# Kernel tuning notes

Hardware: AMD Instinct MI355X
Metric: run time of the kernel (lower is better)

The kernel has to match this reference:

```python
import jax, jax.numpy as jnp
import numpy as np

C = 512; H = 64; W = 64; STRIDE = 16; NA = 9; IMG = 1024
PRE_NMS = 6000; POST_NMS = 300; NMS_T = 0.7; MIN_SIZE = 16.0
BBOX_CLIP = float(np.log(1000.0 / 16.0))  # standard dw/dh clamp for exp() safety


def _make_anchors():
    # 3 scales x 3 aspect ratios on a stride-16 grid -> (H*W*9, 4) xyxy anchors
    scales = np.array([128.0, 256.0, 512.0])
    ratios = np.array([0.5, 1.0, 2.0])
    hs = (scales[:, None] * np.sqrt(ratios)[None, :]).ravel()
    ws = (scales[:, None] / np.sqrt(ratios)[None, :]).ravel()
    yy, xx = np.meshgrid((np.arange(H) + 0.5) * STRIDE, (np.arange(W) + 0.5) * STRIDE, indexing='ij')
    ctr = np.stack([xx.ravel(), yy.ravel()], -1)            # (HW, 2) centers
    wh = np.stack([ws, hs], -1)                              # (9, 2)
    anc = np.concatenate([ctr[:, None, :] - 0.5 * wh[None], ctr[:, None, :] + 0.5 * wh[None]], -1)
    return anc.reshape(-1, 4).astype(np.float32)             # (HW*9, 4)


def setup_inputs() -> dict:
    key = jax.random.key(0)
    k = jax.random.split(key, 4)
    return {
        'feature_map': jax.random.normal(k[0], (1, C, H, W), jnp.float32),
        'anchors': jnp.asarray(_make_anchors()),
        'image_shape': jnp.array([IMG, IMG], jnp.int32),
        'conv1_w': 0.01 * jax.random.normal(k[1], (C, C, 3, 3), jnp.float32),
        'conv1_b': jnp.zeros((C,), jnp.float32),
        'cls_w': 0.01 * jax.random.normal(k[2], (NA, C, 1, 1), jnp.float32),
        'cls_b': jnp.zeros((NA,), jnp.float32),
        'box_w': 0.01 * jax.random.normal(k[3], (NA * 4, C, 1, 1), jnp.float32),
        'box_b': jnp.zeros((NA * 4,), jnp.float32),
    }


def _conv(x, w, b):
    dn = ('NCHW', 'OIHW', 'NCHW')
    return jax.lax.conv_general_dilated(x, w, (1, 1), 'SAME', dimension_numbers=dn) + b[None, :, None, None]


def _decode_boxes(deltas, anchors):
    aw = anchors[:, 2] - anchors[:, 0]
    ah = anchors[:, 3] - anchors[:, 1]
    ax = anchors[:, 0] + 0.5 * aw
    ay = anchors[:, 1] + 0.5 * ah
    dx, dy, dw, dh = deltas[:, 0], deltas[:, 1], deltas[:, 2], deltas[:, 3]
    dw = jnp.minimum(dw, BBOX_CLIP)
    dh = jnp.minimum(dh, BBOX_CLIP)
    px = dx * aw + ax
    py = dy * ah + ay
    pw = jnp.exp(dw) * aw
    ph = jnp.exp(dh) * ah
    return jnp.stack([px - 0.5 * pw, py - 0.5 * ph, px + 0.5 * pw, py + 0.5 * ph], -1)


def _pairwise_iou(a, b):
    area_a = (a[:, 2] - a[:, 0]) * (a[:, 3] - a[:, 1])
    area_b = (b[:, 2] - b[:, 0]) * (b[:, 3] - b[:, 1])
    lt = jnp.maximum(a[:, None, :2], b[None, :, :2])
    rb = jnp.minimum(a[:, None, 2:], b[None, :, 2:])
    wh = jnp.clip(rb - lt, 0.0)
    inter = wh[..., 0] * wh[..., 1]
    union = area_a[:, None] + area_b[None, :] - inter
    return jnp.where(union > 0, inter / union, 0.0)


def reference(feature_map, anchors, image_shape, conv1_w, conv1_b, cls_w, cls_b, box_w, box_b):
    # conv head
    y = jax.nn.relu(_conv(feature_map, conv1_w, conv1_b))
    scores = _conv(y, cls_w, cls_b).reshape(-1)            # (H*W*9,)  torch .view(-1) order
    deltas = _conv(y, box_w, box_b).reshape(-1, 4)         # (H*W*9, 4) torch .reshape(-1,4) order
    preds = _decode_boxes(deltas, anchors)

    # filter_proposals: sigmoid -> topk 6000 -> clamp -> min-size -> NMS(0.7) -> top 300
    s = jax.nn.sigmoid(scores)
    topv, topi = jax.lax.top_k(s, PRE_NMS)                  # sorted descending
    b = preds[topi]
    h_img = image_shape[0].astype(jnp.float32)
    w_img = image_shape[1].astype(jnp.float32)
    b = jnp.stack([jnp.clip(b[:, 0], 0.0, w_img), jnp.clip(b[:, 1], 0.0, h_img),
                   jnp.clip(b[:, 2], 0.0, w_img), jnp.clip(b[:, 3], 0.0, h_img)], -1)
    valid = ((b[:, 2] - b[:, 0]) >= MIN_SIZE) & ((b[:, 3] - b[:, 1]) >= MIN_SIZE)

    iou = _pairwise_iou(b, b)                               # (6000, 6000)
    idx = jnp.arange(PRE_NMS)

    def body(i, keep):  # greedy NMS in score order (boxes already sorted desc)
        sup = (iou[i] > NMS_T) & keep[i] & (idx > i)
        return keep & (~sup)

    keep = jax.lax.fori_loop(0, PRE_NMS, body, valid)
    fs = jnp.where(keep, topv, -1.0)                        # suppressed/invalid -> sentinel
    sc, i2 = jax.lax.top_k(fs, POST_NMS)
    return b[i2], sc
```

## Files before the change

### kernel.cpp

```cpp
#include <hip/hip_runtime.h>
#include <hip/hip_bf16.h>

typedef unsigned int u32;
typedef unsigned long long u64;

#define OFF_Y      0ull
#define OFF_WT     8388608ull
#define OFF_ZPART  8388608ull
#define OFF_SCORES 11337728ull
#define OFF_DRAW   11485184ull
#define OFF_HIST   12075008ull
#define MEMSET_LEN 524288ull
#define OFF_TOPV   12665344ull
#define OFF_BOXES  12714496ull
#define OFF_VW     12812800ull
#define OFF_MASK   12813824ull

#define NS     36864
#define PRE    6000
#define POST   300
#define SORTN  8192
#define MROW   96

__global__ __launch_bounds__(256) void k_wtrans(const float* __restrict__ gw,
                                                float* __restrict__ wT) {
    int o = blockIdx.x * 256 + threadIdx.x;
    if (o >= 512 * 512 * 9) return;
    int ci = o / 4608;
    int r = o - ci * 4608;
    int co = r / 9;
    int k = r - co * 9;
    wT[o] = gw[(co * 512 + ci) * 9 + k];
}

#define CI 16
#define NROW 4
#define XROW 66
#define CHUNK_ELEMS (CI * NROW * XROW)
#define STAGE_IT 17
__global__ __launch_bounds__(256) void k_conv1(const float* __restrict__ x,
                                               const float* __restrict__ wT,
                                               const float* __restrict__ gb,
                                               float* __restrict__ y) {
    __shared__ float xs[CHUNK_ELEMS];
    const int t = threadIdx.x;
    const int tx = t & 63;
    const int wv = __builtin_amdgcn_readfirstlane(t >> 6);
    const int cob = (blockIdx.x & 15) << 5;
    const int h0 = (blockIdx.x >> 4) << 1;
    const int co_base = cob + (wv << 3);

    int offs[STAGE_IT];
    u32 vmask = 0;
#pragma unroll
    for (int u = 0; u < STAGE_IT; ++u) {
        int idx = t + u * 256;
        offs[u] = 0;
        if (idx < CHUNK_ELEMS) {
            int ci = idx / (NROW * XROW);
            int rem = idx - ci * (NROW * XROW);
            int row = rem / XROW;
            int col = rem - row * XROW;
            int gr = h0 + row - 1, gc = col - 1;
            if ((unsigned)gr < 64u && (unsigned)gc < 64u) {
                offs[u] = ci * 4096 + (gr << 6) + gc;
                vmask |= 1u << u;
            }
        }
    }

    float acc[8][2];
#pragma unroll
    for (int c = 0; c < 8; ++c) { acc[c][0] = 0.f; acc[c][1] = 0.f; }

    float st[STAGE_IT];
#pragma unroll
    for (int u = 0; u < STAGE_IT; ++u)
        st[u] = (vmask >> u & 1) ? x[offs[u]] : 0.f;

#pragma unroll 1
    for (int cc = 0; cc < 32; ++cc) {
        if (cc) __syncthreads();
#pragma unroll
        for (int u = 0; u < STAGE_IT; ++u) {
            int idx = t + u * 256;
            if (idx < CHUNK_ELEMS) xs[idx] = st[u];
        }
        __syncthreads();
        if (cc + 1 < 32) {
            const float* xsrc = x + (cc + 1) * CI * 4096;
#pragma unroll
            for (int u = 0; u < STAGE_IT; ++u)
                st[u] = (vmask >> u & 1) ? xsrc[offs[u]] : 0.f;
        }

        const int cig0 = cc * CI;
#pragma unroll 1
        for (int ci = 0; ci < CI; ++ci) {
            float xr[12];
            {
                const float* xp = xs + ci * (NROW * XROW) + tx;
#pragma unroll
                for (int r = 0; r < NROW; ++r) {
                    xr[r * 3 + 0] = xp[r * XROW + 0];
                    xr[r * 3 + 1] = xp[r * XROW + 1];
                    xr[r * 3 + 2] = xp[r * XROW + 2];
                }
            }
            const float* wbase = wT + ((size_t)(cig0 + ci) * 512 + co_base) * 9;
            {
                float4 wq[9];
                const float4* wp = (const float4*)wbase;
#pragma unroll
                for (int i = 0; i < 9; ++i) wq[i] = wp[i];
                const float* w = (const float*)wq;
#pragma unroll
                for (int co = 0; co < 4; ++co)
#pragma unroll
                    for (int k = 0; k < 9; ++k) {
                        const int kh = k / 3, kw = k - kh * 3;
                        float wv_ = w[co * 9 + k];
                        acc[co][0] += wv_ * xr[(0 + kh) * 3 + kw];
                        acc[co][1] += wv_ * xr[(1 + kh) * 3 + kw];
                    }
            }
            {
                float4 wq[9];
                const float4* wp = (const float4*)(wbase + 36);
#pragma unroll
                for (int i = 0; i < 9; ++i) wq[i] = wp[i];
                const float* w = (const float*)wq;
#pragma unroll
                for (int co = 0; co < 4; ++co)
#pragma unroll
                    for (int k = 0; k < 9; ++k) {
                        const int kh = k / 3, kw = k - kh * 3;
                        float wv_ = w[co * 9 + k];
                        acc[co + 4][0] += wv_ * xr[(0 + kh) * 3 + kw];
                        acc[co + 4][1] += wv_ * xr[(1 + kh) * 3 + kw];
                    }
            }
        }
    }

#pragma unroll
    for (int co = 0; co < 8; ++co) {
        float bias = gb[co_base + co];
#pragma unroll
        for (int r = 0; r < 2; ++r) {
            float v = acc[co][r] + bias;
            v = v > 0.f ? v : 0.f;
            y[(co_base + co) * 4096 + ((h0 + r) << 6) + tx] = v;
        }
    }
}

__global__ __launch_bounds__(256) void k_heads_part(const float* __restrict__ y,
                                                    const float* __restrict__ cw,
                                                    const float* __restrict__ bw,
                                                    float* __restrict__ zpart) {
    __shared__ __align__(16) float ys[64][132];
    const int t = threadIdx.x;
    const int px = t & 63;
    const int gu = __builtin_amdgcn_readfirstlane(t >> 6);
    const int px0 = (blockIdx.x & 63) << 6;
    const int q = blockIdx.x >> 6;
    const int cib = q << 7;
    const int nch = (gu == 0) ? 12 : 11;

    const float* wrow[12];
#pragma unroll
    for (int j = 0; j < 12; ++j) {
        int ch = gu + 4 * j;
        if (ch < 9) wrow[j] = cw + ch * 512;
        else if (ch < 45) wrow[j] = bw + (ch - 9) * 512;
        else wrow[j] = cw;
    }
    float acc[12];
#pragma unroll
    for (int j = 0; j < 12; ++j) acc[j] = 0.f;

    for (int idx = t; idx < 128 * 64; idx += 256) {
        int ci = idx >> 6;
        int pp = idx & 63;
        ys[pp][ci] = y[(cib + ci) * 4096 + px0 + pp];
    }
    __syncthreads();

#pragma unroll 1
    for (int cq = 0; cq < 32; ++cq) {
        float4 yv = *(const float4*)&ys[px][cq << 2];
        float4 wv[12];
#pragma unroll
        for (int j = 0; j < 12; ++j)
            if (j < nch) wv[j] = *(const float4*)(wrow[j] + cib + (cq << 2));
#pragma unroll
        for (int j = 0; j < 12; ++j)
            if (j < nch)
                acc[j] += wv[j].x * yv.x + wv[j].y * yv.y + wv[j].z * yv.z + wv[j].w * yv.w;
    }
    for (int j = 0; j < nch; ++j) {
        int ch = gu + 4 * j;
        zpart[((q * 45 + ch) << 12) + px0 + px] = acc[j];
    }
}

__global__ __launch_bounds__(256) void k_hreduce(const float* __restrict__ zpart,
                                                 const float* __restrict__ cb,
                                                 const float* __restrict__ bb,
                                                 float* __restrict__ scores,
                                                 float* __restrict__ draw,
                                                 u32* __restrict__ hist) {
    int i = blockIdx.x * 256 + threadIdx.x;
    if (i >= 45 * 4096) return;
    int ch = i >> 12;
    int sp = i & 4095;
    float z = zpart[((0 * 45 + ch) << 12) + sp] + zpart[((1 * 45 + ch) << 12) + sp] +
              zpart[((2 * 45 + ch) << 12) + sp] + zpart[((3 * 45 + ch) << 12) + sp];
    if (ch < 9) {
        z += cb[ch];
        float s = 1.f / (1.f + expf(-z));
        scores[(ch << 12) + sp] = s;
        u32 sb = __float_as_uint(s);
        atomicAdd(&hist[sb >> 13], 1u);
    } else {
        z += bb[ch - 9];
        draw[((ch - 9) << 12) + sp] = z;
    }
}

__global__ __launch_bounds__(1024) void k_select(const u32* __restrict__ hist,
                                                 const float* __restrict__ scores,
                                                 const float* __restrict__ draw,
                                                 const float* __restrict__ anchors,
                                                 const int* __restrict__ ishape,
                                                 float* __restrict__ boxes,
                                                 float* __restrict__ topv,
                                                 u64* __restrict__ vw) {
    __shared__ u32 csum[1024];
    __shared__ u32 suf[1024];
    __shared__ u64 sk[SORTN];
    __shared__ int sel_s, cnt_s;
    const int t = threadIdx.x;

    u32 s = 0;
    const u32* hp = hist + t * 128;
    for (int i = 0; i < 128; ++i) s += hp[i];
    csum[t] = s;
    suf[t] = s;
    if (t == 0) cnt_s = 0;
    __syncthreads();
    for (int off = 1; off < 1024; off <<= 1) {
        u32 v = suf[t] + ((t + off < 1024) ? suf[t + off] : 0u);
        __syncthreads();
        suf[t] = v;
        __syncthreads();
    }
    u32 above = suf[t] - csum[t];
    if (above < (u32)PRE && suf[t] >= (u32)PRE) {
        u32 run = above;
        int bstar = t * 128;
        u32 found = 0;
        for (int b2 = 127; b2 >= 0; --b2) {
            u32 c = hp[b2];
            if (!found && run + c >= (u32)PRE) { bstar = t * 128 + b2; found = 1; }
            if (!found) run += c;
        }
        sel_s = bstar;
    }
    for (int i = t; i < SORTN; i += 1024) sk[i] = 0;
    __syncthreads();

    const int sel = sel_s;
    for (int i = t; i < NS; i += 1024) {
        u32 sb = __float_as_uint(scores[i]);
        if ((int)(sb >> 13) >= sel) {
            int p = atomicAdd(&cnt_s, 1);
            if (p < SORTN) sk[p] = ((u64)sb << 32) | (u32)(~i);
        }
    }
    __syncthreads();

    const int base = t << 3;
    u64 a[8];
    {
#pragma unroll
        for (int u = 0; u < 8; ++u) a[u] = sk[base + u];
#pragma unroll
        for (int k = 2; k <= 8; k <<= 1) {
#pragma unroll
            for (int j = k >> 1; j > 0; j >>= 1) {
#pragma unroll
                for (int u = 0; u < 8; ++u) {
                    if ((u & j) == 0) {
                        int l = u | j;
                        bool up = (((base + u) & k) == 0);
                        u64 x0 = a[u], x1 = a[l];
                        if (up ? (x0 < x1) : (x0 > x1)) { a[u] = x1; a[l] = x0; }
                    }
                }
            }
        }
#pragma unroll
        for (int u = 0; u < 8; ++u) sk[base + u] = a[u];
        __syncthreads();
    }
    for (int k = 16; k <= SORTN; k <<= 1) {
        for (int j = k >> 1; j >= 8; j >>= 1) {
#pragma unroll
            for (int s2 = 0; s2 < 4; ++s2) {
                int pidx = t + (s2 << 10);
                int i = ((pidx & ~(j - 1)) << 1) | (pidx & (j - 1));
                int l = i | j;
                u64 x0 = sk[i], x1 = sk[l];
                bool up = ((i & k) == 0);
                if (up ? (x0 < x1) : (x0 > x1)) { sk[i] = x1; sk[l] = x0; }
            }
            __syncthreads();
        }
#pragma unroll
        for (int u = 0; u < 8; ++u) a[u] = sk[base + u];
        {
            bool up = ((base & k) == 0);
#pragma unroll
            for (int j = 4; j > 0; j >>= 1) {
#pragma unroll
                for (int u = 0; u < 8; ++u) {
                    if ((u & j) == 0) {
                        int l = u | j;
                        u64 x0 = a[u], x1 = a[l];
                        if (up ? (x0 < x1) : (x0 > x1)) { a[u] = x1; a[l] = x0; }
                    }
                }
            }
        }
#pragma unroll
        for (int u = 0; u < 8; ++u) sk[base + u] = a[u];
        __syncthreads();
    }

    const float wimg = (float)ishape[1], himg = (float)ishape[0];
#pragma unroll 1
    for (int s2 = 0; s2 < 6; ++s2) {
        int r = (s2 << 10) + t;
        bool valid = false;
        if (r < PRE) {
            u64 key = sk[r];
            u32 sb = (u32)(key >> 32);
            int i = (int)(~(u32)key);
            topv[r] = __uint_as_float(sb);
            int c = i >> 10;
            int t4 = i & 1023;
            float4 d4 = *(const float4*)(draw + c * 4096 + (t4 << 2));
            float4 a4 = *(const float4*)(anchors + i * 4);
            float aw = a4.z - a4.x, ah = a4.w - a4.y;
            float ax = a4.x + 0.5f * aw, ay = a4.y + 0.5f * ah;
            const float CLIPV = (float)4.135166556742356;
            float dw = fminf(d4.z, CLIPV);
            float dh = fminf(d4.w, CLIPV);
            float px = d4.x * aw + ax, py = d4.y * ah + ay;
            float pw = expf(dw) * aw, ph = expf(dh) * ah;
            float x1 = fminf(fmaxf(px - 0.5f * pw, 0.f), wimg);
            float y1 = fminf(fmaxf(py - 0.5f * ph, 0.f), himg);
            float x2 = fminf(fmaxf(px + 0.5f * pw, 0.f), wimg);
            float y2 = fminf(fmaxf(py + 0.5f * ph, 0.f), himg);
            valid = (x2 - x1 >= 16.f) && (y2 - y1 >= 16.f);
            *(float4*)(boxes + r * 4) = make_float4(x1, y1, x2, y2);
        }
        u64 bm = __ballot(valid);
        if ((t & 63) == 0) vw[(s2 << 4) + (t >> 6)] = bm;
    }
}

__global__ __launch_bounds__(256) void k_mask(const float* __restrict__ boxes,
                                              u64* __restrict__ mask) {
    __shared__ float4 cbx[16 * 65];
    const int t = threadIdx.x;
    const int r0 = blockIdx.x << 4;
    const int row = r0 + (t >> 4);
    const int wloc = t & 15;
    float4 rb = *(const float4*)(boxes + row * 4);
    float area_a = (rb.z - rb.x) * (rb.w - rb.y);
    for (int chunk = 0; chunk < 6; ++chunk) {
        int j0c = chunk << 10;
        for (int idx = t; idx < 1024; idx += 256) {
            int j = j0c + idx;
            float4 v = make_float4(0.f, 0.f, 0.f, 0.f);
            if (j < PRE) v = *(const float4*)(boxes + j * 4);
            cbx[(idx >> 6) * 65 + (idx & 63)] = v;
        }
        __syncthreads();
        u64 bits = 0;
        const float4* cbr = cbx + wloc * 65;
        for (int b = 0; b < 64; ++b) {
            int j = j0c + (wloc << 6) + b;
            float4 ob = cbr[b];
            float area_b = (ob.z - ob.x) * (ob.w - ob.y);
            float ltx = fmaxf(rb.x, ob.x), lty = fmaxf(rb.y, ob.y);
            float rbx = fminf(rb.z, ob.z), rby = fminf(rb.w, ob.w);
            float wx = fmaxf(rbx - ltx, 0.f), wy = fmaxf(rby - lty, 0.f);
            float inter = wx * wy;
            float uni = area_a + area_b - inter;
            float iou = (uni > 0.f) ? (inter / uni) : 0.f;
            if (iou > 0.7f && j > row && j < PRE) bits |= (1ull << b);
        }
        mask[(size_t)row * MROW + (chunk << 4) + wloc] = bits;
        __syncthreads();
    }
}

__global__ __launch_bounds__(320) void k_nms_out(const u64* __restrict__ mask,
                                                 const u64* __restrict__ vw,
                                                 const float* __restrict__ boxes,
                                                 const float* __restrict__ topv,
                                                 float* __restrict__ out) {
    __shared__ u64 rem[MROW];
    __shared__ u64 rows16[16][MROW];
    __shared__ u64 kws[MROW];
    __shared__ int keepl[POST];
    const int tid = threadIdx.x;
    for (int i = tid; i < MROW; i += 320) { rem[i] = 0ull; kws[i] = 0ull; }
    __syncthreads();
    int kc = 0;
    bool done = false;
    for (int w = 0; w < 94 && !done; ++w) {
        u64 aw = vw[w] & ~rem[w];
        u64 kwbits = 0;
        while (aw != 0ull && !done) {
            int bq[16];
            u64 tmp = aw;
#pragma unroll
            for (int q2 = 0; q2 < 16; ++q2) {
                bq[q2] = tmp ? __builtin_ctzll(tmp) : 64;
                tmp &= tmp - 1;
            }
#pragma unroll
            for (int u = 0; u < 5; ++u) {
                int i = tid + u * 320;
                if (i < 16 * MROW) {
                    int q2 = i / MROW;
                    int ww = i - q2 * MROW;
                    if (bq[q2] < 64)
                        rows16[q2][ww] = mask[(size_t)((w << 6) + bq[q2]) * MROW + ww];
                }
            }
            __syncthreads();
            for (int q2 = 0; q2 < 16; ++q2) {
                int b = bq[q2];
                if (b >= 64) break;
                if (!((aw >> b) & 1ull)) continue;
                if (tid == 0) keepl[kc] = (w << 6) + b;
                kc++;
                kwbits |= (1ull << b);
                if (kc >= POST) { done = true; break; }
                if (tid < MROW) rem[tid] |= rows16[q2][tid];
                aw &= ~rows16[q2][w];
                aw &= ~(1ull << b);
            }
            __syncthreads();
        }
        if (tid == 0) kws[w] = kwbits;
        __syncthreads();
    }
    __syncthreads();

    int j = tid;
    if (j >= POST) return;
    int r;
    float sc;
    if (j < kc) {
        r = keepl[j];
        sc = topv[r];
    } else {
        int target = j - kc;
        r = PRE - 1;
        int cum = 0;
        for (int w = 0; w < 94; ++w) {
            u64 kb = kws[w];
            int nvalid = (w < 93) ? 64 : 48;
            u64 vmask2 = (nvalid == 64) ? ~0ull : ((1ull << nvalid) - 1ull);
            u64 nk = (~kb) & vmask2;
            int c = __popcll(nk);
            if (cum + c > target) {
                int need = target - cum;
                u64 m = nk;
                for (int q = 0; q < need; ++q) m &= (m - 1);
                r = (w << 6) + __builtin_ctzll(m);
                break;
            }
            cum += c;
        }
        sc = -1.0f;
    }
    out[j * 4 + 0] = boxes[r * 4 + 0];
    out[j * 4 + 1] = boxes[r * 4 + 1];
    out[j * 4 + 2] = boxes[r * 4 + 2];
    out[j * 4 + 3] = boxes[r * 4 + 3];
    out[1200 + j] = sc;
}

extern "C" void kernel_launch(void* const* d_in, const int* in_sizes, int n_in,
                              void* d_out, int out_size, void* d_ws, size_t ws_size,
                              hipStream_t stream) {
    const float* x = (const float*)d_in[0];
    const float* anchors = (const float*)d_in[1];
    const int* ishape = (const int*)d_in[2];
    const float* c1w = (const float*)d_in[3];
    const float* c1b = (const float*)d_in[4];
    const float* clw = (const float*)d_in[5];
    const float* clb = (const float*)d_in[6];
    const float* bxw = (const float*)d_in[7];
    const float* bxb = (const float*)d_in[8];

    char* ws = (char*)d_ws;
    float* y      = (float*)(ws + OFF_Y);
    float* wT     = (float*)(ws + OFF_WT);
    float* zpart  = (float*)(ws + OFF_ZPART);
    float* scores = (float*)(ws + OFF_SCORES);
    float* draw   = (float*)(ws + OFF_DRAW);
    u32*   hist   = (u32*)(ws + OFF_HIST);
    float* topv   = (float*)(ws + OFF_TOPV);
    float* boxes  = (float*)(ws + OFF_BOXES);
    u64*   vw     = (u64*)(ws + OFF_VW);
    u64*   mask   = (u64*)(ws + OFF_MASK);

    k_wtrans<<<(512 * 512 * 9 + 255) / 256, 256, 0, stream>>>(c1w, wT);
    k_conv1<<<512, 256, 0, stream>>>(x, wT, c1b, y);
    hipMemsetAsync(ws + OFF_HIST, 0, MEMSET_LEN, stream);
    k_heads_part<<<256, 256, 0, stream>>>(y, clw, bxw, zpart);
    k_hreduce<<<(45 * 4096 + 255) / 256, 256, 0, stream>>>(zpart, clb, bxb, scores, draw, hist);
    k_select<<<1, 1024, 0, stream>>>(hist, scores, draw, anchors, ishape, boxes, topv, vw);
    k_mask<<<PRE / 16, 256, 0, stream>>>(boxes, mask);
    k_nms_out<<<1, 320, 0, stream>>>(mask, vw, boxes, topv, (float*)d_out);
}
```

Baseline: 773.7 us.

## Restructure conv1 to one output row per block with packed FMA weights

The 3x3 conv is reworked so each block handles a single output row instead of two. The grid doubles to 1024 blocks and shared staging shrinks to 3 input rows. The weight transpose now puts the kernel tap outermost, so each thread loads 8 consecutive output-channel weights per tap as float4 pairs and accumulates with 2-wide vector FMAs, aiming at packed FP32 math and fewer loads; launch bounds also request higher occupancy. The histogram memset is folded into k_heads_part to drop a separate memset call. The trade-off is that input rows are now reused across only one output row, so more staged input is loaded per output.

```diff
diff --git a/kernel.cpp b/kernel.cpp
--- a/kernel.cpp
+++ b/kernel.cpp
@@ -3,6 +3,8 @@
 
 typedef unsigned int u32;
 typedef unsigned long long u64;
+typedef float v2f __attribute__((ext_vector_type(2)));
+typedef float v4f __attribute__((ext_vector_type(4)));
 
 #define OFF_Y      0ull
 #define OFF_WT     8388608ull
@@ -10,7 +12,6 @@
 #define OFF_SCORES 11337728ull
 #define OFF_DRAW   11485184ull
 #define OFF_HIST   12075008ull
-#define MEMSET_LEN 524288ull
 #define OFF_TOPV   12665344ull
 #define OFF_BOXES  12714496ull
 #define OFF_VW     12812800ull
@@ -28,26 +29,25 @@
     if (o >= 512 * 512 * 9) return;
     int ci = o / 4608;
     int r = o - ci * 4608;
-    int co = r / 9;
-    int k = r - co * 9;
-    wT[o] = gw[(co * 512 + ci) * 9 + k];
+    int k = r >> 9;
+    int co = r & 511;
+    wT[o] = gw[co * 4608 + ci * 9 + k];
 }
 
 #define CI 16
-#define NROW 4
 #define XROW 66
-#define CHUNK_ELEMS (CI * NROW * XROW)
-#define STAGE_IT 17
-__global__ __launch_bounds__(256) void k_conv1(const float* __restrict__ x,
-                                               const float* __restrict__ wT,
-                                               const float* __restrict__ gb,
-                                               float* __restrict__ y) {
+#define CHUNK_ELEMS (CI * 3 * XROW)
+#define STAGE_IT 13
+__global__ __launch_bounds__(256, 4) void k_conv1(const float* __restrict__ x,
+                                                  const float* __restrict__ wT,
+                                                  const float* __restrict__ gb,
+                                                  float* __restrict__ y) {
     __shared__ float xs[CHUNK_ELEMS];
     const int t = threadIdx.x;
     const int tx = t & 63;
     const int wv = __builtin_amdgcn_readfirstlane(t >> 6);
     const int cob = (blockIdx.x & 15) << 5;
-    const int h0 = (blockIdx.x >> 4) << 1;
+    const int h0 = blockIdx.x >> 4;
     const int co_base = cob + (wv << 3);
 
     int offs[STAGE_IT];
@@ -57,8 +57,8 @@
         int idx = t + u * 256;
         offs[u] = 0;
         if (idx < CHUNK_ELEMS) {
-            int ci = idx / (NROW * XROW);
-            int rem = idx - ci * (NROW * XROW);
+            int ci = idx / (3 * XROW);
+            int rem = idx - ci * (3 * XROW);
             int row = rem / XROW;
             int col = rem - row * XROW;
             int gr = h0 + row - 1, gc = col - 1;
@@ -69,9 +69,9 @@
         }
     }
 
-    float acc[8][2];
-#pragma unroll
-    for (int c = 0; c < 8; ++c) { acc[c][0] = 0.f; acc[c][1] = 0.f; }
+    v2f acc2[4];
+#pragma unroll
+    for (int j = 0; j < 4; ++j) acc2[j] = (v2f){0.f, 0.f};
 
     float st[STAGE_IT];
 #pragma unroll
@@ -95,72 +95,57 @@
         }
 
         const int cig0 = cc * CI;
-#pragma unroll 1
+#pragma unroll 2
         for (int ci = 0; ci < CI; ++ci) {
-            float xr[12];
+            float xr[9];
             {
-                const float* xp = xs + ci * (NROW * XROW) + tx;
-#pragma unroll
-                for (int r = 0; r < NROW; ++r) {
+                const float* xp = xs + ci * (3 * XROW) + tx;
+#pragma unroll
+                for (int r = 0; r < 3; ++r) {
                     xr[r * 3 + 0] = xp[r * XROW + 0];
                     xr[r * 3 + 1] = xp[r * XROW + 1];
                     xr[r * 3 + 2] = xp[r * XROW + 2];
                 }
             }
-            const float* wbase = wT + ((size_t)(cig0 + ci) * 512 + co_base) * 9;
-            {
-                float4 wq[9];
-                const float4* wp = (const float4*)wbase;
-#pragma unroll
-                for (int i = 0; i < 9; ++i) wq[i] = wp[i];
-                const float* w = (const float*)wq;
-#pragma unroll
-                for (int co = 0; co < 4; ++co)
-#pragma unroll
-                    for (int k = 0; k < 9; ++k) {
-                        const int kh = k / 3, kw = k - kh * 3;
-                        float wv_ = w[co * 9 + k];
-                        acc[co][0] += wv_ * xr[(0 + kh) * 3 + kw];
-                        acc[co][1] += wv_ * xr[(1 + kh) * 3 + kw];
-                    }
-            }
-            {
-                float4 wq[9];
-                const float4* wp = (const float4*)(wbase + 36);
-#pragma unroll
-                for (int i = 0; i < 9; ++i) wq[i] = wp[i];
-                const float* w = (const float*)wq;
-#pragma unroll
-                for (int co = 0; co < 4; ++co)
-#pragma unroll
-                    for (int k = 0; k < 9; ++k) {
-                        const int kh = k / 3, kw = k - kh * 3;
-                        float wv_ = w[co * 9 + k];
-                        acc[co + 4][0] += wv_ * xr[(0 + kh) * 3 + kw];
-                        acc[co + 4][1] += wv_ * xr[(1 + kh) * 3 + kw];
-                    }
-            }
-        }
-    }
-
-#pragma unroll
-    for (int co = 0; co < 8; ++co) {
-        float bias = gb[co_base + co];
-#pragma unroll
-        for (int r = 0; r < 2; ++r) {
-            float v = acc[co][r] + bias;
-            v = v > 0.f ? v : 0.f;
-            y[(co_base + co) * 4096 + ((h0 + r) << 6) + tx] = v;
-        }
+            const float* wk = wT + (size_t)(cig0 + ci) * 4608 + co_base;
+#pragma unroll
+            for (int k = 0; k < 9; ++k) {
+                v4f wa = *(const v4f*)(wk + k * 512);
+                v4f wb = *(const v4f*)(wk + k * 512 + 4);
+                float xv = xr[k];
+                v2f xp2 = {xv, xv};
+                acc2[0] = __builtin_elementwise_fma(__builtin_shufflevector(wa, wa, 0, 1), xp2, acc2[0]);
+                acc2[1] = __builtin_elementwise_fma(__builtin_shufflevector(wa, wa, 2, 3), xp2, acc2[1]);
+                acc2[2] = __builtin_elementwise_fma(__builtin_shufflevector(wb, wb, 0, 1), xp2, acc2[2]);
+                acc2[3] = __builtin_elementwise_fma(__builtin_shufflevector(wb, wb, 2, 3), xp2, acc2[3]);
+            }
+        }
+    }
+
+#pragma unroll
+    for (int j = 0; j < 4; ++j) {
+        int co0 = co_base + 2 * j;
+        float v0 = acc2[j].x + gb[co0];
+        float v1 = acc2[j].y + gb[co0 + 1];
+        v0 = v0 > 0.f ? v0 : 0.f;
+        v1 = v1 > 0.f ? v1 : 0.f;
+        y[co0 * 4096 + (h0 << 6) + tx] = v0;
+        y[(co0 + 1) * 4096 + (h0 << 6) + tx] = v1;
     }
 }
 
 __global__ __launch_bounds__(256) void k_heads_part(const float* __restrict__ y,
                                                     const float* __restrict__ cw,
                                                     const float* __restrict__ bw,
-                                                    float* __restrict__ zpart) {
+                                                    float* __restrict__ zpart,
+                                                    u32* __restrict__ hist) {
     __shared__ __align__(16) float ys[64][132];
     const int t = threadIdx.x;
+    {
+        int hb = blockIdx.x << 9;
+        hist[hb + t] = 0u;
+        hist[hb + 256 + t] = 0u;
+    }
     const int px = t & 63;
     const int gu = __builtin_amdgcn_readfirstlane(t >> 6);
     const int px0 = (blockIdx.x & 63) << 6;
@@ -466,13 +451,14 @@
 
     int j = tid;
     if (j >= POST) return;
+    int kc2 = kc;
     int r;
     float sc;
-    if (j < kc) {
+    if (j < kc2) {
         r = keepl[j];
         sc = topv[r];
     } else {
-        int target = j - kc;
+        int target = j - kc2;
         r = PRE - 1;
         int cum = 0;
         for (int w = 0; w < 94; ++w) {
@@ -525,9 +511,8 @@
     u64*   mask   = (u64*)(ws + OFF_MASK);
 
     k_wtrans<<<(512 * 512 * 9 + 255) / 256, 256, 0, stream>>>(c1w, wT);
-    k_conv1<<<512, 256, 0, stream>>>(x, wT, c1b, y);
-    hipMemsetAsync(ws + OFF_HIST, 0, MEMSET_LEN, stream);
-    k_heads_part<<<256, 256, 0, stream>>>(y, clw, bxw, zpart);
+    k_conv1<<<1024, 256, 0, stream>>>(x, wT, c1b, y);
+    k_heads_part<<<256, 256, 0, stream>>>(y, clw, bxw, zpart, hist);
     k_hreduce<<<(45 * 4096 + 255) / 256, 256, 0, stream>>>(zpart, clb, bxb, scores, draw, hist);
     k_select<<<1, 1024, 0, stream>>>(hist, scores, draw, anchors, ishape, boxes, topv, vw);
     k_mask<<<PRE / 16, 256, 0, stream>>>(boxes, mask);
```

New measurement: 712.9 us. -7.9%, faster.
